# Kernel optimization log

Hardware: AMD Instinct MI355X
Metric: run time of the kernel (lower is better)

## Reference

```python
import jax, jax.numpy as jnp
import numpy as np

N = 100000
NFEAT = 256
DIMS = [NFEAT, 512, 256, 128, 64, 64]  # last is nhid=64


def spmm(edge_w, src, dst, h):
    # sparse adj @ h : out[d] = sum_{e: dst[e]==d} edge_w[e] * h[src[e]]
    return jax.ops.segment_sum(edge_w[:, None] * h[src], dst, num_segments=N)


def setup_inputs() -> dict:
    key = jax.random.key(0)
    ks = jax.random.split(key, 16)
    x = jax.random.normal(ks[0], (N, NFEAT), dtype=jnp.float32)
    E = 3200000
    src = jax.random.randint(ks[1], (E,), 0, N, dtype=jnp.int32)
    dst = jax.random.randint(ks[2], (E,), 0, N, dtype=jnp.int32)
    edge_w = jax.random.uniform(ks[3], (E,), dtype=jnp.float32)
    inp = {"x": x, "src": src, "dst": dst, "edge_w": edge_w}
    for i in range(5):
        fan_in, fan_out = DIMS[i], DIMS[i + 1]
        std = 1.0 / np.sqrt(fan_in)
        inp[f"W{i+1}"] = jax.random.uniform(ks[4 + 2 * i], (fan_in, fan_out), minval=-std, maxval=std, dtype=jnp.float32)
        inp[f"b{i+1}"] = jax.random.uniform(ks[5 + 2 * i], (fan_out,), minval=-std, maxval=std, dtype=jnp.float32)
    return inp


def reference(x, src, dst, edge_w, W1, b1, W2, b2, W3, b3, W4, b4, W5, b5):
    # GraphConvolution: adj @ (x @ W) + b ; relu between layers; dropout is
    # inference-mode (no-op). Final layer has no relu.
    h = x
    for W, b, act in ((W1, b1, True), (W2, b2, True), (W3, b3, True), (W4, b4, True), (W5, b5, False)):
        h = spmm(edge_w, src, dst, h @ W) + b
        if act:
            h = jax.nn.relu(h)
    return h
```

## Files before the change

### kernel.cpp

```cpp
#include <hip/hip_runtime.h>


typedef __attribute__((ext_vector_type(8))) short short8;
typedef __attribute__((ext_vector_type(4))) float f32x4;

__device__ __forceinline__ ushort f2bf(float f) {
    unsigned u = __float_as_uint(f);
    u += 0x7FFFu + ((u >> 16) & 1u);
    return (ushort)(u >> 16);
}
__device__ __forceinline__ float bfl(unsigned u) { return __uint_as_float(u << 16); }
__device__ __forceinline__ float bfh(unsigned u) { return __uint_as_float(u & 0xFFFF0000u); }

__device__ __forceinline__ void gl_lds16(const void* g, void* l) {
    __builtin_amdgcn_global_load_lds(
        (const __attribute__((address_space(1))) unsigned*)g,
        (__attribute__((address_space(3))) unsigned*)l, 16, 0, 0);
}

#define RANGES 8
#define EPB 16384
#define HB 2048


__global__ __launch_bounds__(256) void prologue_kernel(
        const int* __restrict__ dst, int* __restrict__ deg, int E,
        const float* __restrict__ x, ushort* __restrict__ xb, int n4,
        const float* W1, const float* W2, const float* W3, const float* W4, const float* W5,
        ushort* T1, ushort* T2, ushort* T3, ushort* T4, ushort* T5) {
    int bid = blockIdx.x;
    if (bid < HB) {
        for (int e = bid * 256 + (int)threadIdx.x; e < E; e += HB * 256)
            atomicAdd(&deg[dst[e]], 1);
        return;
    }
    bid -= HB;
    int XB = (n4 + 255) / 256;
    if (bid < XB) {
        int i = bid * 256 + threadIdx.x;
        if (i >= n4) return;
        float4 v = reinterpret_cast<const float4*>(x)[i];
        uint2 o;
        o.x = ((unsigned)f2bf(v.y) << 16) | (unsigned)f2bf(v.x);
        o.y = ((unsigned)f2bf(v.w) << 16) | (unsigned)f2bf(v.z);
        reinterpret_cast<uint2*>(xb)[i] = o;
        return;
    }
    bid -= XB;
    int i = bid * 256 + threadIdx.x;
    const float* W; ushort* T; int K, M, base;
    if      (i < 131072) { W = W1; T = T1; K = 256; M = 512; base = 0; }
    else if (i < 262144) { W = W2; T = T2; K = 512; M = 256; base = 131072; }
    else if (i < 294912) { W = W3; T = T3; K = 256; M = 128; base = 262144; }
    else if (i < 303104) { W = W4; T = T4; K = 128; M = 64;  base = 294912; }
    else if (i < 307200) { W = W5; T = T5; K = 64;  M = 64;  base = 303104; }
    else return;
    int l = i - base;
    int k = l / M, m = l - k * M;
    T[(size_t)m * K + k] = f2bf(W[l]);
}


__global__ __launch_bounds__(256) void scan_p1(const int* __restrict__ deg,
                                               int* __restrict__ sums, int n) {
    int i = blockIdx.x * 256 + threadIdx.x;
    int v = (i < n) ? deg[i] : 0;
    for (int off = 32; off > 0; off >>= 1) v += __shfl_down(v, off, 64);
    __shared__ int ws[4];
    if ((threadIdx.x & 63) == 0) ws[threadIdx.x >> 6] = v;
    __syncthreads();
    if (threadIdx.x == 0) sums[blockIdx.x] = ws[0] + ws[1] + ws[2] + ws[3];
}

__global__ __launch_bounds__(512) void scan_p2(int* __restrict__ sums,
                                               int* __restrict__ rowptr, int n, int nb) {
    __shared__ int sh[512];
    int v = ((int)threadIdx.x < nb) ? sums[threadIdx.x] : 0;
    sh[threadIdx.x] = v;
    __syncthreads();
    for (int off = 1; off < 512; off <<= 1) {
        int t = ((int)threadIdx.x >= off) ? sh[threadIdx.x - off] : 0;
        __syncthreads();
        sh[threadIdx.x] += t;
        __syncthreads();
    }
    if ((int)threadIdx.x < nb) sums[threadIdx.x] = sh[threadIdx.x] - v;
    if (threadIdx.x == 0) rowptr[n] = sh[511];
}

__global__ __launch_bounds__(256) void scan_p3(const int* __restrict__ deg,
                                               const int* __restrict__ sums,
                                               int* __restrict__ rowptr,
                                               int* __restrict__ pos, int n) {
    __shared__ int sh[256];
    int i = blockIdx.x * 256 + threadIdx.x;
    int v = (i < n) ? deg[i] : 0;
    sh[threadIdx.x] = v;
    __syncthreads();
    for (int off = 1; off < 256; off <<= 1) {
        int t = ((int)threadIdx.x >= off) ? sh[threadIdx.x - off] : 0;
        __syncthreads();
        sh[threadIdx.x] += t;
        __syncthreads();
    }
    int excl = sums[blockIdx.x] + sh[threadIdx.x] - v;
    if (i < n) { rowptr[i] = excl; pos[i] = excl; }
}

__global__ __launch_bounds__(256) void scatter_part(const int* __restrict__ src,
                                                    const int* __restrict__ dst,
                                                    const float* __restrict__ ew,
                                                    int* pos,
                                                    unsigned* __restrict__ erec,
                                                    int E, int rspan) {
    int range = blockIdx.x & (RANGES - 1);
    int chunk = blockIdx.x / RANGES;
    int lo = range * rspan;
    int base = chunk * EPB;
    int lim = base + EPB < E ? base + EPB : E;
    for (int e = base + (int)threadIdx.x; e < lim; e += 256) {
        int d = dst[e];
        if (d >= lo && d < lo + rspan) {
            int p = atomicAdd(&pos[d], 1);
            float w = ew[e];
            unsigned w15 = (unsigned)(w * 32768.0f + 0.5f);
            if (w15 > 32767u) w15 = 32767u;
            erec[p] = ((unsigned)src[e] << 15) | w15;
        }
    }
}


#define EDGE_FMA(r, v)                                            \
    {                                                             \
        float w = (float)((r) & 32767u) * (1.0f / 32768.0f);      \
        acc[0] = fmaf(w, bfl((v).x), acc[0]);                     \
        acc[1] = fmaf(w, bfh((v).x), acc[1]);                     \
        acc[2] = fmaf(w, bfl((v).y), acc[2]);                     \
        acc[3] = fmaf(w, bfh((v).y), acc[3]);                     \
        acc[4] = fmaf(w, bfl((v).z), acc[4]);                     \
        acc[5] = fmaf(w, bfh((v).z), acc[5]);                     \
        acc[6] = fmaf(w, bfl((v).w), acc[6]);                     \
        acc[7] = fmaf(w, bfh((v).w), acc[7]);                     \
    }

template <int FAN, bool OUTF32>
__global__ __launch_bounds__(256) void spmm_gather_bf(
        const ushort* __restrict__ T, const int* __restrict__ rowptr,
        const unsigned* __restrict__ erec, const float* __restrict__ bias,
        void* __restrict__ outp, int N, int doRelu) {
    constexpr int LPR = FAN / 8;
    int g = blockIdx.x * 256 + threadIdx.x;
    int row = g / LPR;
    int lane = g - row * LPR;
    if (row >= N) return;
    const int beg = rowptr[row];
    const int end = rowptr[row + 1];
    float acc[8];
#pragma unroll
    for (int j = 0; j < 8; ++j) acc[j] = 0.0f;

    const ushort* Tl = T + lane * 8;
    int p = beg;
    for (; p + 8 <= end; p += 8) {
        unsigned rr[8];
        uint4 vv[8];
#pragma unroll
        for (int u = 0; u < 8; ++u) rr[u] = erec[p + u];
#pragma unroll
        for (int u = 0; u < 8; ++u)
            vv[u] = *reinterpret_cast<const uint4*>(Tl + (size_t)(rr[u] >> 15) * FAN);
#pragma unroll
        for (int u = 0; u < 8; ++u) EDGE_FMA(rr[u], vv[u]);
    }
    for (; p < end; ++p) {
        unsigned r0 = erec[p];
        uint4 v0 = *reinterpret_cast<const uint4*>(Tl + (size_t)(r0 >> 15) * FAN);
        EDGE_FMA(r0, v0);
    }
    if (bias != nullptr) {
#pragma unroll
        for (int j = 0; j < 8; ++j) acc[j] += bias[lane * 8 + j];
    }
    if (doRelu) {
#pragma unroll
        for (int j = 0; j < 8; ++j) acc[j] = fmaxf(acc[j], 0.0f);
    }
    if (OUTF32) {
        float* o = (float*)outp + (size_t)row * FAN + lane * 8;
        *reinterpret_cast<float4*>(o)     = make_float4(acc[0], acc[1], acc[2], acc[3]);
        *reinterpret_cast<float4*>(o + 4) = make_float4(acc[4], acc[5], acc[6], acc[7]);
    } else {
        uint4 u;
        u.x = ((unsigned)f2bf(acc[1]) << 16) | (unsigned)f2bf(acc[0]);
        u.y = ((unsigned)f2bf(acc[3]) << 16) | (unsigned)f2bf(acc[2]);
        u.z = ((unsigned)f2bf(acc[5]) << 16) | (unsigned)f2bf(acc[4]);
        u.w = ((unsigned)f2bf(acc[7]) << 16) | (unsigned)f2bf(acc[6]);
        *reinterpret_cast<uint4*>((ushort*)outp + (size_t)row * FAN + lane * 8) = u;
    }
}


template <int BN, int WM, int WN>
__global__ __launch_bounds__(256) void gemm_mfma(const ushort* __restrict__ A,
                                                 const ushort* __restrict__ BT,
                                                 const float* __restrict__ bias,
                                                 ushort* __restrict__ C,
                                                 int N, int K, int M, int doBiasRelu) {
    constexpr int BM = 128, BK = 64;
    constexpr int WROWS = BM / WM;
    constexpr int WCOLS = BN / WN;
    constexpr int MR = WROWS / 16;
    constexpr int NR = WCOLS / 16;
    constexpr int AISS = (BM * BK / 8) / 256;
    constexpr int BISS = (BN * BK / 8) / 256;
    __shared__ ushort As[BM][BK];
    __shared__ ushort Bs[BN][BK];

    const int tid  = threadIdx.x;
    const int wid  = tid >> 6;
    const int lane = tid & 63;
    const int l16  = lane & 15;
    const int lq   = lane >> 4;
    const int wr   = wid / WN;
    const int wc   = wid % WN;
    const long row0 = (long)blockIdx.x * BM;
    const int  col0 = blockIdx.y * BN;

    f32x4 acc[MR][NR] = {};

    for (int k0 = 0; k0 < K; k0 += BK) {
#pragma unroll
        for (int j = 0; j < AISS; ++j) {
            int t  = (wid * AISS + j) * 64 + lane;
            int r  = t >> 3;
            int cw = t & 7;
            const ushort* g = A + (row0 + r) * K + k0 + ((cw ^ (r & 7)) << 3);
            gl_lds16(g, (char*)&As[0][0] + (size_t)t * 16);
        }
#pragma unroll
        for (int j = 0; j < BISS; ++j) {
            int t  = (wid * BISS + j) * 64 + lane;
            int r  = t >> 3;
            int cw = t & 7;
            const ushort* g = BT + (size_t)(col0 + r) * K + k0 + ((cw ^ (r & 7)) << 3);
            gl_lds16(g, (char*)&Bs[0][0] + (size_t)t * 16);
        }
        __syncthreads();

        short8 af[2][MR], bf[2][NR];
#pragma unroll
        for (int kk = 0; kk < 2; ++kk) {
#pragma unroll
            for (int m = 0; m < MR; ++m) {
                int r = wr * WROWS + m * 16 + l16;
                af[kk][m] = *reinterpret_cast<const short8*>(&As[r][((kk * 4 + lq) ^ (r & 7)) * 8]);
            }
#pragma unroll
            for (int n = 0; n < NR; ++n) {
                int r = wc * WCOLS + n * 16 + l16;
                bf[kk][n] = *reinterpret_cast<const short8*>(&Bs[r][((kk * 4 + lq) ^ (r & 7)) * 8]);
            }
        }
#pragma unroll
        for (int kk = 0; kk < 2; ++kk)
#pragma unroll
            for (int m = 0; m < MR; ++m)
#pragma unroll
                for (int n = 0; n < NR; ++n)
                    acc[m][n] = __builtin_amdgcn_mfma_f32_16x16x32_bf16(af[kk][m], bf[kk][n], acc[m][n], 0, 0, 0);
        __syncthreads();
    }

#pragma unroll
    for (int m = 0; m < MR; ++m) {
#pragma unroll
        for (int n = 0; n < NR; ++n) {
            int gcol = col0 + wc * WCOLS + n * 16 + l16;
            float bb = doBiasRelu ? bias[gcol] : 0.0f;
#pragma unroll
            for (int r = 0; r < 4; ++r) {
                long grow = row0 + wr * WROWS + m * 16 + lq * 4 + r;
                if (grow < N) {
                    float f = acc[m][n][r] + bb;
                    if (doBiasRelu) f = fmaxf(f, 0.0f);
                    C[grow * M + gcol] = f2bf(f);
                }
            }
        }
    }
}


extern "C" void kernel_launch(void* const* d_in, const int* in_sizes, int n_in,
                              void* d_out, int out_size, void* d_ws, size_t ws_size,
                              hipStream_t stream) {
    const float* x   = (const float*)d_in[0];
    const int*   src = (const int*)d_in[1];
    const int*   dst = (const int*)d_in[2];
    const float* ew  = (const float*)d_in[3];
    const float* W[5]  = {(const float*)d_in[4], (const float*)d_in[6], (const float*)d_in[8],
                          (const float*)d_in[10], (const float*)d_in[12]};
    const float* b[5]  = {(const float*)d_in[5], (const float*)d_in[7], (const float*)d_in[9],
                          (const float*)d_in[11], (const float*)d_in[13]};
    const int Kd[5] = {256, 512, 256, 128, 64};
    const int Md[5] = {512, 256, 128, 64, 64};

    const int N = in_sizes[0] / 256;
    const int E = in_sizes[1];
    const int Npad = ((N + 127) / 128) * 128;
    const int nb = (N + 255) / 256;

    char*  ws  = (char*)d_ws;
    size_t off = 0;
    ushort* buf0 = (ushort*)(ws + off); off += (size_t)Npad * 512 * 2;
    ushort* buf1 = (ushort*)(ws + off); off += (size_t)Npad * 512 * 2;
    ushort* xb   = (ushort*)(ws + off); off += (size_t)Npad * 256 * 2;
    int* rowptr  = (int*)(ws + off);    off += ((size_t)N + 1) * 4;
    int* deg     = (int*)(ws + off);    off += (size_t)N * 4;
    int* pos     = (int*)(ws + off);    off += (size_t)N * 4;
    int* sums    = (int*)(ws + off);    off += 512 * 4;
    off = (off + 15) & ~(size_t)15;
    unsigned* erec = (unsigned*)(ws + off); off += (size_t)E * 4;
    ushort* WT[5];
    for (int i = 0; i < 5; ++i) { WT[i] = (ushort*)(ws + off); off += (size_t)Kd[i] * Md[i] * 2; }
    (void)ws_size; (void)n_in; (void)out_size;

    const int nchunks = (E + EPB - 1) / EPB;
    const int rspan   = (N + RANGES - 1) / RANGES;
    const int n4 = N * 64;
    const int XB = (n4 + 255) / 256;
    const int WB = (307200 + 255) / 256;

    hipMemsetAsync(deg, 0, (size_t)N * 4, stream);
    prologue_kernel<<<HB + XB + WB, 256, 0, stream>>>(
        dst, deg, E, x, xb, n4,
        W[0], W[1], W[2], W[3], W[4], WT[0], WT[1], WT[2], WT[3], WT[4]);
    scan_p1<<<nb, 256, 0, stream>>>(deg, sums, N);
    scan_p2<<<1, 512, 0, stream>>>(sums, rowptr, N, nb);
    scan_p3<<<nb, 256, 0, stream>>>(deg, sums, rowptr, pos, N);
    scatter_part<<<RANGES * nchunks, 256, 0, stream>>>(src, dst, ew, pos, erec, E, rspan);

    spmm_gather_bf<256, false><<<((size_t)N * 32 + 255) / 256, 256, 0, stream>>>(
        xb, rowptr, erec, nullptr, buf0, N, 0);
    {
        dim3 g(Npad / 128, 512 / 128);
        gemm_mfma<128, 2, 2><<<g, 256, 0, stream>>>(buf0, WT[0], b[0], buf1, N, 256, 512, 1);
    }
    {
        dim3 g(Npad / 128, 256 / 128);
        gemm_mfma<128, 2, 2><<<g, 256, 0, stream>>>(buf1, WT[1], nullptr, buf0, N, 512, 256, 0);
    }
    spmm_gather_bf<256, false><<<((size_t)N * 32 + 255) / 256, 256, 0, stream>>>(
        buf0, rowptr, erec, b[1], buf1, N, 1);
    {
        dim3 g(Npad / 128, 1);
        gemm_mfma<128, 2, 2><<<g, 256, 0, stream>>>(buf1, WT[2], nullptr, buf0, N, 256, 128, 0);
    }
    spmm_gather_bf<128, false><<<((size_t)N * 16 + 255) / 256, 256, 0, stream>>>(
        buf0, rowptr, erec, b[2], buf1, N, 1);
    {
        dim3 g(Npad / 128, 1);
        gemm_mfma<64, 4, 1><<<g, 256, 0, stream>>>(buf1, WT[3], nullptr, buf0, N, 128, 64, 0);
    }
    spmm_gather_bf<64, false><<<((size_t)N * 8 + 255) / 256, 256, 0, stream>>>(
        buf0, rowptr, erec, b[3], buf1, N, 1);
    {
        dim3 g(Npad / 128, 1);
        gemm_mfma<64, 4, 1><<<g, 256, 0, stream>>>(buf1, WT[4], nullptr, buf0, N, 64, 64, 0);
    }
    spmm_gather_bf<64, true><<<((size_t)N * 8 + 255) / 256, 256, 0, stream>>>(
        buf0, rowptr, erec, b[4], (float*)d_out, N, 0);
}
```

Baseline: 1.212 ms.

## Fuse small next-layer GEMMs into SpMM gather epilogue and add nontemporal memory hints

The 128-to-64 and 64-to-64 dense projections now run inside the SpMM gather kernel. Each block stages its aggregated rows in LDS and multiplies them by the next weight matrix, which it converts to bf16 in LDS. This removes two GEMM launches and the round trip of the intermediate activations through global memory. Streaming loads and stores (edge lists, erec, outputs) are also marked nontemporal to reduce cache pollution. In exchange, every block re-reads and converts the full weight matrix, and the extra syncthreads and LDS use may lower occupancy of the gather.

```diff
diff --git a/kernel.cpp b/kernel.cpp
--- a/kernel.cpp
+++ b/kernel.cpp
@@ -3,6 +3,9 @@
 
 typedef __attribute__((ext_vector_type(8))) short short8;
 typedef __attribute__((ext_vector_type(4))) float f32x4;
+typedef __attribute__((ext_vector_type(2))) unsigned uint2n;
+typedef __attribute__((ext_vector_type(4))) unsigned uint4n;
+typedef __attribute__((ext_vector_type(4))) float float4n;
 
 __device__ __forceinline__ ushort f2bf(float f) {
     unsigned u = __float_as_uint(f);
@@ -26,12 +29,12 @@
 __global__ __launch_bounds__(256) void prologue_kernel(
         const int* __restrict__ dst, int* __restrict__ deg, int E,
         const float* __restrict__ x, ushort* __restrict__ xb, int n4,
-        const float* W1, const float* W2, const float* W3, const float* W4, const float* W5,
-        ushort* T1, ushort* T2, ushort* T3, ushort* T4, ushort* T5) {
+        const float* W1, const float* W2, const float* W3,
+        ushort* T1, ushort* T2, ushort* T3) {
     int bid = blockIdx.x;
     if (bid < HB) {
         for (int e = bid * 256 + (int)threadIdx.x; e < E; e += HB * 256)
-            atomicAdd(&deg[dst[e]], 1);
+            atomicAdd(&deg[__builtin_nontemporal_load(&dst[e])], 1);
         return;
     }
     bid -= HB;
@@ -39,11 +42,11 @@
     if (bid < XB) {
         int i = bid * 256 + threadIdx.x;
         if (i >= n4) return;
-        float4 v = reinterpret_cast<const float4*>(x)[i];
-        uint2 o;
+        float4n v = __builtin_nontemporal_load(&reinterpret_cast<const float4n*>(x)[i]);
+        uint2n o;
         o.x = ((unsigned)f2bf(v.y) << 16) | (unsigned)f2bf(v.x);
         o.y = ((unsigned)f2bf(v.w) << 16) | (unsigned)f2bf(v.z);
-        reinterpret_cast<uint2*>(xb)[i] = o;
+        __builtin_nontemporal_store(o, &reinterpret_cast<uint2n*>(xb)[i]);
         return;
     }
     bid -= XB;
@@ -52,8 +55,6 @@
     if      (i < 131072) { W = W1; T = T1; K = 256; M = 512; base = 0; }
     else if (i < 262144) { W = W2; T = T2; K = 512; M = 256; base = 131072; }
     else if (i < 294912) { W = W3; T = T3; K = 256; M = 128; base = 262144; }
-    else if (i < 303104) { W = W4; T = T4; K = 128; M = 64;  base = 294912; }
-    else if (i < 307200) { W = W5; T = T5; K = 64;  M = 64;  base = 303104; }
     else return;
     int l = i - base;
     int k = l / M, m = l - k * M;
@@ -119,13 +120,14 @@
     int base = chunk * EPB;
     int lim = base + EPB < E ? base + EPB : E;
     for (int e = base + (int)threadIdx.x; e < lim; e += 256) {
-        int d = dst[e];
+        int d = __builtin_nontemporal_load(&dst[e]);
         if (d >= lo && d < lo + rspan) {
             int p = atomicAdd(&pos[d], 1);
-            float w = ew[e];
+            float w = __builtin_nontemporal_load(&ew[e]);
             unsigned w15 = (unsigned)(w * 32768.0f + 0.5f);
             if (w15 > 32767u) w15 = 32767u;
-            erec[p] = ((unsigned)src[e] << 15) | w15;
+            unsigned s = (unsigned)__builtin_nontemporal_load(&src[e]);
+            __builtin_nontemporal_store((s << 15) | w15, &erec[p]);
         }
     }
 }
@@ -144,59 +146,127 @@
         acc[7] = fmaf(w, bfh((v).w), acc[7]);                     \
     }
 
-template <int FAN, bool OUTF32>
+template <int FAN, int MOUT, bool OUTF32>
 __global__ __launch_bounds__(256) void spmm_gather_bf(
         const ushort* __restrict__ T, const int* __restrict__ rowptr,
         const unsigned* __restrict__ erec, const float* __restrict__ bias,
-        void* __restrict__ outp, int N, int doRelu) {
-    constexpr int LPR = FAN / 8;
-    int g = blockIdx.x * 256 + threadIdx.x;
-    int row = g / LPR;
-    int lane = g - row * LPR;
-    if (row >= N) return;
-    const int beg = rowptr[row];
-    const int end = rowptr[row + 1];
+        const float* __restrict__ Wnext, void* __restrict__ outp,
+        int N, int doRelu) {
+    constexpr int LPR  = FAN / 8;
+    constexpr int ROWS = 256 / LPR;
+    __shared__ float  hrow[(MOUT > 0) ? ROWS : 1][(MOUT > 0) ? (FAN + 4) : 1];
+    __shared__ ushort Wl[(MOUT > 0) ? FAN : 1][(MOUT > 0) ? MOUT : 1];
+
+    const int grp  = threadIdx.x / LPR;
+    const int lane = threadIdx.x % LPR;
+    const int row  = blockIdx.x * ROWS + grp;
+    const bool active = row < N;
+
+    if constexpr (MOUT > 0) {
+        for (int i = threadIdx.x; i < FAN * MOUT; i += 256)
+            Wl[i / MOUT][i % MOUT] = f2bf(Wnext[i]);
+    }
+
     float acc[8];
 #pragma unroll
     for (int j = 0; j < 8; ++j) acc[j] = 0.0f;
 
-    const ushort* Tl = T + lane * 8;
-    int p = beg;
-    for (; p + 8 <= end; p += 8) {
-        unsigned rr[8];
-        uint4 vv[8];
-#pragma unroll
-        for (int u = 0; u < 8; ++u) rr[u] = erec[p + u];
-#pragma unroll
-        for (int u = 0; u < 8; ++u)
-            vv[u] = *reinterpret_cast<const uint4*>(Tl + (size_t)(rr[u] >> 15) * FAN);
-#pragma unroll
-        for (int u = 0; u < 8; ++u) EDGE_FMA(rr[u], vv[u]);
-    }
-    for (; p < end; ++p) {
-        unsigned r0 = erec[p];
-        uint4 v0 = *reinterpret_cast<const uint4*>(Tl + (size_t)(r0 >> 15) * FAN);
-        EDGE_FMA(r0, v0);
-    }
-    if (bias != nullptr) {
-#pragma unroll
-        for (int j = 0; j < 8; ++j) acc[j] += bias[lane * 8 + j];
-    }
-    if (doRelu) {
-#pragma unroll
-        for (int j = 0; j < 8; ++j) acc[j] = fmaxf(acc[j], 0.0f);
-    }
-    if (OUTF32) {
-        float* o = (float*)outp + (size_t)row * FAN + lane * 8;
-        *reinterpret_cast<float4*>(o)     = make_float4(acc[0], acc[1], acc[2], acc[3]);
-        *reinterpret_cast<float4*>(o + 4) = make_float4(acc[4], acc[5], acc[6], acc[7]);
+    if (active) {
+        const int beg = __builtin_nontemporal_load(&rowptr[row]);
+        const int end = __builtin_nontemporal_load(&rowptr[row + 1]);
+        const ushort* Tl = T + lane * 8;
+        int p = beg;
+        for (; p + 8 <= end; p += 8) {
+            unsigned rr[8];
+            uint4 vv[8];
+#pragma unroll
+            for (int u = 0; u < 8; ++u) rr[u] = __builtin_nontemporal_load(&erec[p + u]);
+#pragma unroll
+            for (int u = 0; u < 8; ++u)
+                vv[u] = *reinterpret_cast<const uint4*>(Tl + (size_t)(rr[u] >> 15) * FAN);
+#pragma unroll
+            for (int u = 0; u < 8; ++u) EDGE_FMA(rr[u], vv[u]);
+        }
+        for (; p < end; ++p) {
+            unsigned r0 = __builtin_nontemporal_load(&erec[p]);
+            uint4 v0 = *reinterpret_cast<const uint4*>(Tl + (size_t)(r0 >> 15) * FAN);
+            EDGE_FMA(r0, v0);
+        }
+        if (bias != nullptr) {
+#pragma unroll
+            for (int j = 0; j < 8; ++j) acc[j] += bias[lane * 8 + j];
+        }
+        if (doRelu) {
+#pragma unroll
+            for (int j = 0; j < 8; ++j) acc[j] = fmaxf(acc[j], 0.0f);
+        }
+    }
+
+    if constexpr (MOUT > 0) {
+#pragma unroll
+        for (int j = 0; j < 8; ++j) hrow[grp][lane * 8 + j] = acc[j];
+        __syncthreads();
+        constexpr int MPL = (MOUT * ROWS) / 256;
+        constexpr int TPR = 256 / ROWS;
+        const int orow = threadIdx.x / TPR;
+        const int m0   = (threadIdx.x % TPR) * MPL;
+        float t[MPL];
+#pragma unroll
+        for (int j = 0; j < MPL; ++j) t[j] = 0.0f;
+        for (int k = 0; k < FAN; ++k) {
+            float hk = hrow[orow][k];
+            if constexpr (MPL == 4) {
+                uint2 w = *reinterpret_cast<const uint2*>(&Wl[k][m0]);
+                t[0] = fmaf(hk, bfl(w.x), t[0]);
+                t[1] = fmaf(hk, bfh(w.x), t[1]);
+                t[2] = fmaf(hk, bfl(w.y), t[2]);
+                t[3] = fmaf(hk, bfh(w.y), t[3]);
+            } else {
+                uint4 w = *reinterpret_cast<const uint4*>(&Wl[k][m0]);
+                t[0] = fmaf(hk, bfl(w.x), t[0]);
+                t[1] = fmaf(hk, bfh(w.x), t[1]);
+                t[2] = fmaf(hk, bfl(w.y), t[2]);
+                t[3] = fmaf(hk, bfh(w.y), t[3]);
+                t[4] = fmaf(hk, bfl(w.z), t[4]);
+                t[5] = fmaf(hk, bfh(w.z), t[5]);
+                t[6] = fmaf(hk, bfl(w.w), t[6]);
+                t[7] = fmaf(hk, bfh(w.w), t[7]);
+            }
+        }
+        int og = blockIdx.x * ROWS + orow;
+        if (og < N) {
+            ushort* o = (ushort*)outp + (size_t)og * MOUT + m0;
+            if constexpr (MPL == 4) {
+                uint2n u;
+                u.x = ((unsigned)f2bf(t[1]) << 16) | (unsigned)f2bf(t[0]);
+                u.y = ((unsigned)f2bf(t[3]) << 16) | (unsigned)f2bf(t[2]);
+                __builtin_nontemporal_store(u, reinterpret_cast<uint2n*>(o));
+            } else {
+                uint4n u;
+                u.x = ((unsigned)f2bf(t[1]) << 16) | (unsigned)f2bf(t[0]);
+                u.y = ((unsigned)f2bf(t[3]) << 16) | (unsigned)f2bf(t[2]);
+                u.z = ((unsigned)f2bf(t[5]) << 16) | (unsigned)f2bf(t[4]);
+                u.w = ((unsigned)f2bf(t[7]) << 16) | (unsigned)f2bf(t[6]);
+                __builtin_nontemporal_store(u, reinterpret_cast<uint4n*>(o));
+            }
+        }
     } else {
-        uint4 u;
-        u.x = ((unsigned)f2bf(acc[1]) << 16) | (unsigned)f2bf(acc[0]);
-        u.y = ((unsigned)f2bf(acc[3]) << 16) | (unsigned)f2bf(acc[2]);
-        u.z = ((unsigned)f2bf(acc[5]) << 16) | (unsigned)f2bf(acc[4]);
-        u.w = ((unsigned)f2bf(acc[7]) << 16) | (unsigned)f2bf(acc[6]);
-        *reinterpret_cast<uint4*>((ushort*)outp + (size_t)row * FAN + lane * 8) = u;
+        if (!active) return;
+        if (OUTF32) {
+            float* o = (float*)outp + (size_t)row * FAN + lane * 8;
+            float4n f0 = {acc[0], acc[1], acc[2], acc[3]};
+            float4n f1 = {acc[4], acc[5], acc[6], acc[7]};
+            __builtin_nontemporal_store(f0, reinterpret_cast<float4n*>(o));
+            __builtin_nontemporal_store(f1, reinterpret_cast<float4n*>(o + 4));
+        } else {
+            uint4n u;
+            u.x = ((unsigned)f2bf(acc[1]) << 16) | (unsigned)f2bf(acc[0]);
+            u.y = ((unsigned)f2bf(acc[3]) << 16) | (unsigned)f2bf(acc[2]);
+            u.z = ((unsigned)f2bf(acc[5]) << 16) | (unsigned)f2bf(acc[4]);
+            u.w = ((unsigned)f2bf(acc[7]) << 16) | (unsigned)f2bf(acc[6]);
+            __builtin_nontemporal_store(
+                u, reinterpret_cast<uint4n*>((ushort*)outp + (size_t)row * FAN + lane * 8));
+        }
     }
 }
 
@@ -322,27 +392,26 @@
     int* sums    = (int*)(ws + off);    off += 512 * 4;
     off = (off + 15) & ~(size_t)15;
     unsigned* erec = (unsigned*)(ws + off); off += (size_t)E * 4;
-    ushort* WT[5];
-    for (int i = 0; i < 5; ++i) { WT[i] = (ushort*)(ws + off); off += (size_t)Kd[i] * Md[i] * 2; }
+    ushort* WT[3];
+    for (int i = 0; i < 3; ++i) { WT[i] = (ushort*)(ws + off); off += (size_t)Kd[i] * Md[i] * 2; }
     (void)ws_size; (void)n_in; (void)out_size;
 
     const int nchunks = (E + EPB - 1) / EPB;
     const int rspan   = (N + RANGES - 1) / RANGES;
     const int n4 = N * 64;
     const int XB = (n4 + 255) / 256;
-    const int WB = (307200 + 255) / 256;
+    const int WB = (294912 + 255) / 256;
 
     hipMemsetAsync(deg, 0, (size_t)N * 4, stream);
     prologue_kernel<<<HB + XB + WB, 256, 0, stream>>>(
-        dst, deg, E, x, xb, n4,
-        W[0], W[1], W[2], W[3], W[4], WT[0], WT[1], WT[2], WT[3], WT[4]);
+        dst, deg, E, x, xb, n4, W[0], W[1], W[2], WT[0], WT[1], WT[2]);
     scan_p1<<<nb, 256, 0, stream>>>(deg, sums, N);
     scan_p2<<<1, 512, 0, stream>>>(sums, rowptr, N, nb);
     scan_p3<<<nb, 256, 0, stream>>>(deg, sums, rowptr, pos, N);
     scatter_part<<<RANGES * nchunks, 256, 0, stream>>>(src, dst, ew, pos, erec, E, rspan);
 
-    spmm_gather_bf<256, false><<<((size_t)N * 32 + 255) / 256, 256, 0, stream>>>(
-        xb, rowptr, erec, nullptr, buf0, N, 0);
+    spmm_gather_bf<256, 0, false><<<((size_t)N * 32 + 255) / 256, 256, 0, stream>>>(
+        xb, rowptr, erec, nullptr, nullptr, buf0, N, 0);
     {
         dim3 g(Npad / 128, 512 / 128);
         gemm_mfma<128, 2, 2><<<g, 256, 0, stream>>>(buf0, WT[0], b[0], buf1, N, 256, 512, 1);
@@ -351,24 +420,16 @@
         dim3 g(Npad / 128, 256 / 128);
         gemm_mfma<128, 2, 2><<<g, 256, 0, stream>>>(buf1, WT[1], nullptr, buf0, N, 512, 256, 0);
     }
-    spmm_gather_bf<256, false><<<((size_t)N * 32 + 255) / 256, 256, 0, stream>>>(
-        buf0, rowptr, erec, b[1], buf1, N, 1);
+    spmm_gather_bf<256, 0, false><<<((size_t)N * 32 + 255) / 256, 256, 0, stream>>>(
+        buf0, rowptr, erec, b[1], nullptr, buf1, N, 1);
     {
         dim3 g(Npad / 128, 1);
         gemm_mfma<128, 2, 2><<<g, 256, 0, stream>>>(buf1, WT[2], nullptr, buf0, N, 256, 128, 0);
     }
-    spmm_gather_bf<128, false><<<((size_t)N * 16 + 255) / 256, 256, 0, stream>>>(
-        buf0, rowptr, erec, b[2], buf1, N, 1);
-    {
-        dim3 g(Npad / 128, 1);
-        gemm_mfma<64, 4, 1><<<g, 256, 0, stream>>>(buf1, WT[3], nullptr, buf0, N, 128, 64, 0);
-    }
-    spmm_gather_bf<64, false><<<((size_t)N * 8 + 255) / 256, 256, 0, stream>>>(
-        buf0, rowptr, erec, b[3], buf1, N, 1);
-    {
-        dim3 g(Npad / 128, 1);
-        gemm_mfma<64, 4, 1><<<g, 256, 0, stream>>>(buf1, WT[4], nullptr, buf0, N, 64, 64, 0);
-    }
-    spmm_gather_bf<64, true><<<((size_t)N * 8 + 255) / 256, 256, 0, stream>>>(
-        buf0, rowptr, erec, b[4], (float*)d_out, N, 0);
-}
+    spmm_gather_bf<128, 64, false><<<((size_t)N * 16 + 255) / 256, 256, 0, stream>>>(
+        buf0, rowptr, erec, b[2], W[3], buf1, N, 1);
+    spmm_gather_bf<64, 64, false><<<((size_t)N * 8 + 255) / 256, 256, 0, stream>>>(
+        buf1, rowptr, erec, b[3], W[4], buf0, N, 1);
+    spmm_gather_bf<64, 0, true><<<((size_t)N * 8 + 255) / 256, 256, 0, stream>>>(
+        buf0, rowptr, erec, b[4], nullptr, (float*)d_out, N, 0);
+}
```

After: 1.260 ms. 4.0% more time.
